# Kernel tuning notes

Hardware: AMD Instinct MI355X
Metric: run time of the kernel (lower is better)

The kernel has to match this reference:

```python
import jax, jax.numpy as jnp
import numpy as np
import math

HEAD_NUM = 16


def _split_qkv(qkv, head_num):
    # torch: rearrange(qkv, 'b t (d k h) -> k b h t d', k=3, h=head_num)
    B, T, E3 = qkv.shape
    d = E3 // (3 * head_num)
    qkv = qkv.reshape(B, T, d, 3, head_num)        # (b,t,d,k,h)
    qkv = jnp.transpose(qkv, (3, 0, 4, 1, 2))       # (k,b,h,t,d)
    return qkv[0], qkv[1], qkv[2]


def setup_inputs() -> dict:
    key = jax.random.key(0)
    ks = jax.random.split(key, 6)
    B, T, E = 4, 1024, 1024
    return {
        "x": jax.random.normal(ks[0], (B, T, E), dtype=jnp.float32),
        "y": jax.random.normal(ks[1], (B, T, E), dtype=jnp.float32),
        "Wqkv1": jax.random.normal(ks[2], (3 * E, E), dtype=jnp.float32) * 0.02,
        "Wqkv2": jax.random.normal(ks[3], (3 * E, E), dtype=jnp.float32) * 0.02,
        "Wout1": jax.random.normal(ks[4], (E, E), dtype=jnp.float32) * 0.02,
        "Wout2": jax.random.normal(ks[5], (E, E), dtype=jnp.float32) * 0.02,
    }


def reference(x, y, Wqkv1, Wqkv2, Wout1, Wout2):
    B, T, E = x.shape
    H = HEAD_NUM
    dk = math.sqrt(E / H)

    qkv1 = x @ Wqkv1.T                              # (B,T,3E)
    qkv2 = y @ Wqkv2.T
    q1, k1, v1 = _split_qkv(qkv1, H)                # each (B,H,T,d)
    q2, k2, v2 = _split_qkv(qkv2, H)

    # cross attention: stream-2 queries attend to stream-1 keys/values and vice versa
    energy1 = jnp.einsum('bhid,bhjd->bhij', q2, k1) / dk
    energy2 = jnp.einsum('bhid,bhjd->bhij', q1, k2) / dk
    attn1 = jax.nn.softmax(energy1, axis=-1)
    attn2 = jax.nn.softmax(energy2, axis=-1)

    xo = jnp.einsum('bhij,bhjd->bhid', attn1, v1)   # (B,H,T,d)
    yo = jnp.einsum('bhij,bhjd->bhid', attn2, v2)
    xo = jnp.transpose(xo, (0, 2, 1, 3)).reshape(B, T, E)  # b t (h d)
    yo = jnp.transpose(yo, (0, 2, 1, 3)).reshape(B, T, E)

    return xo @ Wout1.T, yo @ Wout2.T
```

## Files before the change

kernel.cpp:

```cpp
#include <hip/hip_runtime.h>
#include <hip/hip_bf16.h>

typedef __hip_bfloat16 bf16;
typedef __attribute__((ext_vector_type(8))) short short8;
typedef __attribute__((ext_vector_type(4))) short short4v;
typedef __attribute__((ext_vector_type(4))) float f32x4;

#define MFMA_BF16(a, b, c) __builtin_amdgcn_mfma_f32_16x16x32_bf16((a), (b), (c), 0, 0, 0)

#define QSCALE 0.1803368860111270f

__device__ __forceinline__ short f2bf(float f) {
    union { bf16 h; short s; } u;
    u.h = __float2bfloat16(f);
    return u.s;
}

#if defined(__has_builtin) && __has_builtin(__builtin_amdgcn_cvt_pk_bf16_f32)
typedef __attribute__((ext_vector_type(2))) __bf16 bf16x2_t;
__device__ __forceinline__ unsigned int pk2(float a, float b) {
    union { bf16x2_t v; unsigned int u; } x;
    x.v = __builtin_amdgcn_cvt_pk_bf16_f32(a, b);
    return x.u;
}
#else
__device__ __forceinline__ unsigned int pk2(float a, float b) {
    union { bf16 h[2]; unsigned int u; } x;
    x.h[0] = __float2bfloat16(a);
    x.h[1] = __float2bfloat16(b);
    return x.u;
}
#endif

__device__ __forceinline__ void gload16(const void* g, void* l) {
    __builtin_amdgcn_global_load_lds(
        (const __attribute__((address_space(1))) unsigned int*)g,
        (__attribute__((address_space(3))) unsigned int*)l, 16, 0, 0);
}

__global__ void cvt_fused(const float* __restrict__ x, const float* __restrict__ y,
                          const float* __restrict__ wo1, const float* __restrict__ wo2,
                          const float* __restrict__ wq1, const float* __restrict__ wq2,
                          bf16* __restrict__ ox, bf16* __restrict__ oy,
                          bf16* __restrict__ oo1, bf16* __restrict__ oo2,
                          bf16* __restrict__ oq1, bf16* __restrict__ oq2) {
    const int yb = blockIdx.y;
    if (yb < 4) {
        int i = blockIdx.x * 256 + threadIdx.x;
        const float* src; bf16* dst; int n4;
        switch (yb) {
            case 0:  src = x;   dst = ox;  n4 = 1048576; break;
            case 1:  src = y;   dst = oy;  n4 = 1048576; break;
            case 2:  src = wo1; dst = oo1; n4 = 262144;  break;
            default: src = wo2; dst = oo2; n4 = 262144;  break;
        }
        if (i >= n4) return;
        float4 f = reinterpret_cast<const float4*>(src)[i];
        short4v s;
        s.x = f2bf(f.x); s.y = f2bf(f.y); s.z = f2bf(f.z); s.w = f2bf(f.w);
        reinterpret_cast<short4v*>(dst)[i] = s;
    } else {
        const int np = blockIdx.x;
        if (np >= 3072) return;
        const int comp = np >> 10, rem = np & 1023, h = rem >> 6, d = rem & 63;
        const int srow = d * 48 + comp * 16 + h;
        const float* src = ((yb == 5) ? wq2 : wq1) + (long)srow * 1024;
        bf16* dst = ((yb == 5) ? oq2 : oq1) + (long)np * 1024;
        const float sc = (comp == 0) ? QSCALE : 1.0f;
        int t = threadIdx.x;
        float4 f = reinterpret_cast<const float4*>(src)[t];
        short4v s;
        s.x = f2bf(f.x * sc); s.y = f2bf(f.y * sc); s.z = f2bf(f.z * sc); s.w = f2bf(f.w * sc);
        reinterpret_cast<short4v*>(dst)[t] = s;
    }
}

#define GATE4 do { asm volatile("s_waitcnt vmcnt(4)" ::: "memory"); \
    __builtin_amdgcn_s_barrier(); __builtin_amdgcn_sched_barrier(0); } while (0)

__global__ __launch_bounds__(512, 2)
void gemm_qkv256(const bf16* __restrict__ A0g, const bf16* __restrict__ B0g,
                 void* o0a, void* o0b, void* o0c,
                 const bf16* __restrict__ A1g, const bf16* __restrict__ B1g,
                 void* o1a, void* o1b, void* o1c) {
    extern __shared__ short smem[];
    const int z = blockIdx.z;
    const short* A = reinterpret_cast<const short*>(z ? A1g : A0g);
    const short* B = reinterpret_cast<const short*>(z ? B1g : B0g);
    const int tid  = threadIdx.x;
    const int lane = tid & 63;
    const int w    = tid >> 6;
    const int quad = lane >> 4;
    const int l16  = lane & 15;
    const long M0 = (long)blockIdx.y * 256;
    const long N0 = (long)blockIdx.x * 256;

    const int rowblk = (w >> 2) * 64;
    const int colblk = (w & 3) * 32;
    const int cA0  = (quad ^ (l16 & 7)) * 8;
    const int aoff = (rowblk + l16) * 64;
    const int boff = 16384 + (colblk + l16) * 64;
    const int w512 = w * 512;

    const short* Asrc = A + (M0 + w * 8 + (lane >> 3)) * 1024 + ((lane & 7) ^ (lane >> 3)) * 8;
    const short* Bsrc = B + (N0 + w * 8 + (lane >> 3)) * 1024 + ((lane & 7) ^ (lane >> 3)) * 8;

    f32x4 acc[4][4][2] = {};
    short8 af[4][2], bfv[2][2];

#define SA256(half, tt, nbase) do { \
    const short* _s = Asrc + (half) * 131072 + (tt) * 64; \
    short* _d = smem + (nbase) + (half) * 8192 + w512; \
    gload16(_s, _d); gload16(_s + 65536, _d + 4096); } while (0)
#define SB256(half, tt, nbase) do { \
    const short* _s = Bsrc + (half) * 131072 + (tt) * 64; \
    short* _d = smem + (nbase) + 16384 + (half) * 8192 + w512; \
    gload16(_s, _d); gload16(_s + 65536, _d + 4096); } while (0)
#define RDA256(Ah, bbv) do { \
    _Pragma("unroll") for (int mt = 0; mt < 4; ++mt) { \
        const short* _p = &smem[(bbv) + (Ah) * 8192 + aoff + mt * 1024]; \
        af[mt][0] = *reinterpret_cast<const short8*>(_p + cA0); \
        af[mt][1] = *reinterpret_cast<const short8*>(_p + (cA0 ^ 32)); } } while (0)
#define RDB256(Bh, bbv) do { \
    _Pragma("unroll") for (int nt = 0; nt < 2; ++nt) { \
        const short* _p = &smem[(bbv) + (Bh) * 8192 + boff + nt * 1024]; \
        bfv[nt][0] = *reinterpret_cast<const short8*>(_p + cA0); \
        bfv[nt][1] = *reinterpret_cast<const short8*>(_p + (cA0 ^ 32)); } } while (0)
#define MM256(p) do { \
    __builtin_amdgcn_s_setprio(1); \
    _Pragma("unroll") for (int mt = 0; mt < 4; ++mt) \
    _Pragma("unroll") for (int nt = 0; nt < 2; ++nt) { \
        acc[p][mt][nt] = MFMA_BF16(af[mt][0], bfv[nt][0], acc[p][mt][nt]); \
        acc[p][mt][nt] = MFMA_BF16(af[mt][1], bfv[nt][1], acc[p][mt][nt]); } \
    __builtin_amdgcn_s_setprio(0); } while (0)

    SA256(0, 0, 0); SB256(0, 0, 0); SB256(1, 0, 0); SA256(1, 0, 0);

#pragma unroll 1
    for (int t = 0; t < 15; ++t) {
        const int bb = (t & 1) << 15;
        const int nb = bb ^ 32768;
        GATE4;
        SA256(0, t + 1, nb);
        RDA256(0, bb); RDB256(0, bb);
        __builtin_amdgcn_sched_barrier(0);
        MM256(0);
        GATE4;
        SB256(0, t + 1, nb);
        RDB256(1, bb);
        __builtin_amdgcn_sched_barrier(0);
        MM256(1);
        GATE4;
        SB256(1, t + 1, nb);
        RDA256(1, bb); RDB256(0, bb);
        __builtin_amdgcn_sched_barrier(0);
        MM256(2);
        SA256(1, t + 1, nb);
        RDB256(1, bb);
        __builtin_amdgcn_sched_barrier(0);
        MM256(3);
    }
    asm volatile("s_waitcnt vmcnt(0)" ::: "memory");
    __builtin_amdgcn_s_barrier();
    __builtin_amdgcn_sched_barrier(0);
    {
        const int bb = 32768;
        RDA256(0, bb); RDB256(0, bb); MM256(0);
        RDB256(1, bb); MM256(1);
        RDA256(1, bb); RDB256(0, bb); MM256(2);
        RDB256(1, bb); MM256(3);
    }

    if (blockIdx.x < 8) {
        short* dst = reinterpret_cast<short*>(blockIdx.x < 4 ? (z ? o1a : o0a)
                                                             : (z ? o1b : o0b));
        const int b = (int)(M0 >> 10);
        const int t00 = ((int)M0 & 1023);
        const int hd00 = ((int)blockIdx.x & 3) * 256;
#pragma unroll
        for (int p = 0; p < 4; ++p) {
            const int Ah = p >> 1, Bh = p & 1;
            const int tr0 = t00 + Ah * 128 + rowblk + quad * 4;
#pragma unroll
            for (int nt = 0; nt < 2; ++nt) {
                const int hd = hd00 + Bh * 128 + colblk + nt * 16 + l16;
                const int h = hd >> 6, d = hd & 63;
                short* dp = dst + (long)(b * 16 + h) * 65536 + d;
#pragma unroll
                for (int mt = 0; mt < 4; ++mt)
#pragma unroll
                    for (int r = 0; r < 4; ++r)
                        dp[(long)(tr0 + mt * 16 + r) * 64] = f2bf(acc[p][mt][nt][r]);
            }
        }
    } else {
        short* vT = reinterpret_cast<short*>(z ? o1c : o0c);
        const int b = (int)(M0 >> 10);
        const int hd00 = ((int)blockIdx.x - 8) * 256;
        short* ws = smem + w * 2304;
        const int c8 = (lane & 7) * 8;
        const int colr = lane >> 3;
#pragma unroll
        for (int p = 0; p < 4; ++p) {
            const int Ah = p >> 1, Bh = p & 1;
#pragma unroll
            for (int nt = 0; nt < 2; ++nt)
#pragma unroll
                for (int mt = 0; mt < 4; ++mt) {
                    uint2 uu;
                    uu.x = pk2(acc[p][mt][nt][0], acc[p][mt][nt][1]);
                    uu.y = pk2(acc[p][mt][nt][2], acc[p][mt][nt][3]);
                    *reinterpret_cast<uint2*>(&ws[(nt * 16 + l16) * 72 + mt * 16 + quad * 4]) = uu;
                }
            const int tb = ((int)M0 & 1023) + Ah * 128 + rowblk + c8;
#pragma unroll
            for (int q4 = 0; q4 < 4; ++q4) {
                const int col = q4 * 8 + colr;
                const int hd = hd00 + Bh * 128 + colblk + col;
                const int h = hd >> 6, d = hd & 63;
                short8 v = *reinterpret_cast<const short8*>(&ws[col * 72 + c8]);
                *reinterpret_cast<short8*>(&vT[(long)(b * 16 + h) * 65536 + (long)d * 1024 + tb]) = v;
            }
        }
    }
#undef SA256
#undef SB256
#undef RDA256
#undef RDB256
#undef MM256
}

template <int MODE>
__global__ __launch_bounds__(256)
void gemm_k(const bf16* __restrict__ A0g, const bf16* __restrict__ B0g,
            void* o0a, void* o0b, void* o0c,
            const bf16* __restrict__ A1g, const bf16* __restrict__ B1g,
            void* o1a, void* o1b, void* o1c, int N) {
    __shared__ short smem2[20480];
    const int z = blockIdx.z;
    const short* A = reinterpret_cast<const short*>(z ? A1g : A0g);
    const short* B = reinterpret_cast<const short*>(z ? B1g : B0g);
    const int tid  = threadIdx.x;
    const int lane = tid & 63;
    const int w    = tid >> 6;
    const int wr   = w >> 1;
    const int wc   = w & 1;
    const int quad = lane >> 4;
    const int l16  = lane & 15;
    const long bM = (long)blockIdx.y * 128;

    f32x4 acc[4][4] = {};

    const int sr  = lane >> 2;
    const int scs = ((lane & 3) ^ (sr & 3)) * 8;
    const short* Ag0 = A + (bM + 32 * w + sr) * 1024 + scs;
    const short* Ag1 = Ag0 + 16 * 1024;
    const short* Bg0 = B + ((long)blockIdx.x * 128 + 32 * w + sr) * 1024 + scs;
    const short* Bg1 = Bg0 + 16 * 1024;
    const int sq = (quad ^ (l16 & 3)) * 8;

    {
        short* sb = smem2;
        gload16(Ag0, sb + w * 1024);
        gload16(Ag1, sb + w * 1024 + 512);
        gload16(Bg0, sb + 4096 + w * 1024);
        gload16(Bg1, sb + 4096 + w * 1024 + 512);
    }
    __syncthreads();

    for (int iter = 0; iter < 32; ++iter) {
        const int cur = iter & 1;
        if (iter < 31) {
            const int koff = (iter + 1) * 32;
            short* sb = smem2 + (cur ^ 1) * 8192;
            gload16(Ag0 + koff, sb + w * 1024);
            gload16(Ag1 + koff, sb + w * 1024 + 512);
            gload16(Bg0 + koff, sb + 4096 + w * 1024);
            gload16(Bg1 + koff, sb + 4096 + w * 1024 + 512);
        }
        const short* Ab = smem2 + cur * 8192;
        const short* Bb = Ab + 4096;

        short8 af[4], bfr[4];
#pragma unroll
        for (int mt = 0; mt < 4; ++mt)
            af[mt] = *reinterpret_cast<const short8*>(&Ab[(wr * 64 + mt * 16 + l16) * 32 + sq]);
#pragma unroll
        for (int nt = 0; nt < 4; ++nt)
            bfr[nt] = *reinterpret_cast<const short8*>(&Bb[(wc * 64 + nt * 16 + l16) * 32 + sq]);
#pragma unroll
        for (int mt = 0; mt < 4; ++mt)
#pragma unroll
            for (int nt = 0; nt < 4; ++nt)
                acc[mt][nt] = MFMA_BF16(af[mt], bfr[nt], acc[mt][nt]);

        __syncthreads();
    }

    if (MODE == 1) {
        float* C = reinterpret_cast<float*>(z ? o1a : o0a);
        const long crow = bM + wr * 64 + quad * 4;
        const long ccol = (long)blockIdx.x * 128 + wc * 64 + l16;
#pragma unroll
        for (int mt = 0; mt < 4; ++mt)
#pragma unroll
            for (int nt = 0; nt < 4; ++nt)
#pragma unroll
                for (int r = 0; r < 4; ++r)
                    C[(crow + mt * 16 + r) * (long)N + ccol + nt * 16] = acc[mt][nt][r];
        return;
    }
    if (blockIdx.x < 16) {
        short* dst = reinterpret_cast<short*>(blockIdx.x >= 8 ? (z ? o1b : o0b)
                                                              : (z ? o1a : o0a));
        const int hd0 = (int)(blockIdx.x & 7) * 128 + wc * 64;
        const int b = (int)(bM >> 10);
        const int t0 = ((int)bM & 1023) + wr * 64 + quad * 4;
#pragma unroll
        for (int nt = 0; nt < 4; ++nt) {
            const int hd = hd0 + nt * 16 + l16;
            const int h = hd >> 6, d = hd & 63;
            short* dp = dst + ((long)(b * 16 + h) * 1024) * 64 + d;
#pragma unroll
            for (int mt = 0; mt < 4; ++mt)
#pragma unroll
                for (int r = 0; r < 4; ++r)
                    dp[(long)(t0 + mt * 16 + r) * 64] = f2bf(acc[mt][nt][r]);
        }
    }
}

__global__ __launch_bounds__(256)
void attn_kernel(const bf16* __restrict__ q0g, const bf16* __restrict__ k0g,
                 const bf16* __restrict__ v0g, bf16* __restrict__ o0g,
                 const bf16* __restrict__ q1g, const bf16* __restrict__ k1g,
                 const bf16* __restrict__ v1g, bf16* __restrict__ o1g) {
    __shared__ short smem[16384];
    const int bh = blockIdx.x;
    const int qt = blockIdx.y;
    const int z = blockIdx.z;
    const int b = bh >> 4, h = bh & 15;
    const int tid = threadIdx.x, lane = tid & 63, w = tid >> 6;
    const int quad = lane >> 4, l16 = lane & 15;

    const short* Qb = reinterpret_cast<const short*>(z ? q1g : q0g) + (long)bh * 1024 * 64;
    const short* Kb = reinterpret_cast<const short*>(z ? k1g : k0g) + (long)bh * 1024 * 64;
    const short* Vb = reinterpret_cast<const short*>(z ? v1g : v0g) + (long)bh * 64 * 1024;
    short* Ob = reinterpret_cast<short*>(z ? o1g : o0g);

    short8 qb[2][2];
#pragma unroll
    for (int qg = 0; qg < 2; ++qg) {
        const short* Qp = Qb + (long)(qt * 128 + qg * 64 + w * 16 + l16) * 64;
        qb[qg][0] = *reinterpret_cast<const short8*>(Qp + quad * 8);
        qb[qg][1] = *reinterpret_cast<const short8*>(Qp + 32 + quad * 8);
    }

    const int r8  = lane >> 3;
    const int sc0 = ((lane & 7) ^ (r8 & 3)) * 8;
    const short* Kg0 = Kb + (long)(16 * w + r8) * 64 + sc0;
    const short* Kg1 = Kb + (long)(16 * w + 8 + r8) * 64 + (sc0 ^ 32);
    const short* Vg0 = Vb + (long)(16 * w + r8) * 1024 + sc0;
    const short* Vg1 = Vb + (long)(16 * w + 8 + r8) * 1024 + (sc0 ^ 32);

    const int jbase = 8 * (l16 >> 2) + (l16 & 3);
    const int fKs = (l16 & 3) | (((l16 >> 2) & 1) << 2);
    const int s0  = (quad ^ fKs) * 8;
    const int fVs = (l16 & 3) | (((l16 >> 3) & 1) << 2);
    const int sv  = (quad ^ fVs) * 8;

    f32x4 o[2][4] = {};
    float li[2] = {0.f, 0.f};

    gload16(Kg0, smem + w * 1024); gload16(Kg1, smem + w * 1024 + 512);
    gload16(Vg0, smem + 4096 + w * 1024); gload16(Vg1, smem + 4096 + w * 1024 + 512);

#pragma unroll 1
    for (int iter = 0; iter < 16; ++iter) {
        const int cur = iter & 1;
        short* sb = smem + (cur ^ 1) * 8192;
        const bool pre = iter < 15;
        if (pre) {
            const long ko = (long)(iter + 1) * 4096;
            gload16(Kg0 + ko, sb + w * 1024);
            gload16(Kg1 + ko, sb + w * 1024 + 512);
        }
        if (pre) { asm volatile("s_waitcnt vmcnt(4)" ::: "memory"); }
        else     { asm volatile("s_waitcnt vmcnt(2)" ::: "memory"); }
        __builtin_amdgcn_s_barrier();
        __builtin_amdgcn_sched_barrier(0);

        const short* Ks = smem + cur * 8192;
        const short* Vs = Ks + 4096;

        f32x4 st[2][4];
        __builtin_amdgcn_s_setprio(1);
#pragma unroll
        for (int g = 0; g < 4; ++g) {
            const int goff = (g >> 1) * 32 + (g & 1) * 4;
            const short* kr = Ks + (jbase + goff) * 64;
            short8 k0 = *reinterpret_cast<const short8*>(kr + s0);
            short8 k1 = *reinterpret_cast<const short8*>(kr + (s0 ^ 32));
#pragma unroll
            for (int qg = 0; qg < 2; ++qg) {
                f32x4 zf = {0.f, 0.f, 0.f, 0.f};
                zf = MFMA_BF16(k0, qb[qg][0], zf);
                zf = MFMA_BF16(k1, qb[qg][1], zf);
                st[qg][g] = zf;
            }
        }
        __builtin_amdgcn_s_setprio(0);

        if (pre) {
            const long vo = (long)(iter + 1) * 64;
            gload16(Vg0 + vo, sb + 4096 + w * 1024);
            gload16(Vg1 + vo, sb + 4096 + w * 1024 + 512);
        }

        union { unsigned int u[4]; short8 s; } f0[2], f1[2];
#pragma unroll
        for (int qg = 0; qg < 2; ++qg) {
            float p[4][4];
            float rs = 0.f;
#pragma unroll
            for (int g = 0; g < 4; ++g)
#pragma unroll
                for (int r = 0; r < 4; ++r) {
                    float e = exp2f(st[qg][g][r]);
                    p[g][r] = e;
                    rs += e;
                }
            li[qg] += rs;
            f0[qg].u[0] = pk2(p[0][0], p[0][1]); f0[qg].u[1] = pk2(p[0][2], p[0][3]);
            f0[qg].u[2] = pk2(p[1][0], p[1][1]); f0[qg].u[3] = pk2(p[1][2], p[1][3]);
            f1[qg].u[0] = pk2(p[2][0], p[2][1]); f1[qg].u[1] = pk2(p[2][2], p[2][3]);
            f1[qg].u[2] = pk2(p[3][0], p[3][1]); f1[qg].u[3] = pk2(p[3][2], p[3][3]);
        }

        if (pre) { asm volatile("s_waitcnt vmcnt(4)" ::: "memory"); }
        else     { asm volatile("s_waitcnt vmcnt(0)" ::: "memory"); }
        __builtin_amdgcn_s_barrier();
        __builtin_amdgcn_sched_barrier(0);

        __builtin_amdgcn_s_setprio(1);
#pragma unroll
        for (int dt = 0; dt < 4; ++dt) {
            const short* vr = Vs + (dt * 16 + l16) * 64;
            short8 v0 = *reinterpret_cast<const short8*>(vr + sv);
            short8 v1 = *reinterpret_cast<const short8*>(vr + (sv ^ 32));
#pragma unroll
            for (int qg = 0; qg < 2; ++qg) {
                o[qg][dt] = MFMA_BF16(v0, f0[qg].s, o[qg][dt]);
                o[qg][dt] = MFMA_BF16(v1, f1[qg].s, o[qg][dt]);
            }
        }
        __builtin_amdgcn_s_setprio(0);
    }

    __syncthreads();

#pragma unroll
    for (int qg = 0; qg < 2; ++qg) {
        li[qg] += __shfl_xor(li[qg], 16);
        li[qg] += __shfl_xor(li[qg], 32);
    }

#pragma unroll
    for (int qg = 0; qg < 2; ++qg) {
        short* Os = smem + qg * 5120 + w * 1280;
        const float rl = 1.0f / li[qg];
#pragma unroll
        for (int dt = 0; dt < 4; ++dt) {
            uint2 uu;
            uu.x = pk2(o[qg][dt][0] * rl, o[qg][dt][1] * rl);
            uu.y = pk2(o[qg][dt][2] * rl, o[qg][dt][3] * rl);
            *reinterpret_cast<uint2*>(&Os[l16 * 80 + dt * 16 + quad * 4]) = uu;
        }
#pragma unroll
        for (int p = 0; p < 2; ++p) {
            int row = p * 8 + (lane >> 3);
            int ch = (lane & 7) * 8;
            short8 v = *reinterpret_cast<const short8*>(&Os[row * 80 + ch]);
            *reinterpret_cast<short8*>(&Ob[((long)(b * 1024) + qt * 128 + qg * 64 + w * 16 + row) * 1024 + h * 64 + ch]) = v;
        }
    }
}

extern "C" void kernel_launch(void* const* d_in, const int* in_sizes, int n_in,
                              void* d_out, int out_size, void* d_ws, size_t ws_size,
                              hipStream_t stream) {
    const float* x     = (const float*)d_in[0];
    const float* y     = (const float*)d_in[1];
    const float* Wqkv1 = (const float*)d_in[2];
    const float* Wqkv2 = (const float*)d_in[3];
    const float* Wout1 = (const float*)d_in[4];
    const float* Wout2 = (const float*)d_in[5];

    char* ws = (char*)d_ws;
    bf16* Wqkv1b = (bf16*)(ws + 0);
    bf16* Wqkv2b = (bf16*)(ws + 6291456);
    bf16* Wout1b = (bf16*)(ws + 12582912);
    bf16* Wout2b = (bf16*)(ws + 14680064);
    bf16* xb     = (bf16*)(ws + 16777216);
    bf16* yb     = (bf16*)(ws + 25165824);
    bf16* q1     = (bf16*)(ws + 33554432);
    bf16* k1     = (bf16*)(ws + 41943040);
    bf16* v1T    = (bf16*)(ws + 50331648);
    bf16* q2     = (bf16*)(ws + 58720256);
    bf16* k2     = (bf16*)(ws + 67108864);
    bf16* v2T    = (bf16*)(ws + 75497472);
    bf16* xo     = xb;
    bf16* yo     = yb;

    static bool s_attr = false;
    if (!s_attr) {
        (void)hipFuncSetAttribute(reinterpret_cast<const void*>(&gemm_qkv256),
                                  hipFuncAttributeMaxDynamicSharedMemorySize, 131072);
        s_attr = true;
    }

    cvt_fused<<<dim3(4096, 6), 256, 0, stream>>>(x, y, Wout1, Wout2, Wqkv1, Wqkv2,
                                                 xb, yb, Wout1b, Wout2b, Wqkv1b, Wqkv2b);

    gemm_qkv256<<<dim3(12, 16, 2), 512, 131072, stream>>>(xb, Wqkv1b, q1, k1, v1T,
                                                          yb, Wqkv2b, q2, k2, v2T);

    attn_kernel<<<dim3(64, 8, 2), 256, 0, stream>>>(q2, k1, v1T, xo,
                                                    q1, k2, v2T, yo);

    gemm_k<1><<<dim3(8, 32, 2), 256, 0, stream>>>(xo, Wout1b, (float*)d_out, nullptr, nullptr,
                                                  yo, Wout2b, ((float*)d_out) + 4194304, nullptr, nullptr,
                                                  1024);
}
```

Measured before the change: 263.9 us.

## Switch attention and output GEMM to triple-buffered LDS with one barrier per iteration

Both the attention kernel and the output-projection GEMM move from double-buffered LDS with two sync points per loop to a three-slot ring buffer. Each iteration now issues the next tile's loads first, waits on the previous ones and uses a single barrier. The three slots let the prefetch target a buffer no wave is still reading, which removes the trailing __syncthreads. The GEMM's MFMA block also gets raised priority, and exp2f is replaced with the hardware exp2 builtin. The cost is 50% more shared memory per block, which may lower occupancy.

```diff
diff --git a/kernel.cpp b/kernel.cpp
--- a/kernel.cpp
+++ b/kernel.cpp
@@ -30,6 +30,12 @@
     x.h[1] = __float2bfloat16(b);
     return x.u;
 }
+#endif
+
+#if defined(__has_builtin) && __has_builtin(__builtin_amdgcn_exp2f)
+#define EXP2F(x) __builtin_amdgcn_exp2f(x)
+#else
+#define EXP2F(x) exp2f(x)
 #endif
 
 __device__ __forceinline__ void gload16(const void* g, void* l) {
@@ -230,13 +236,10 @@
 #undef MM256
 }
 
-template <int MODE>
 __global__ __launch_bounds__(256)
-void gemm_k(const bf16* __restrict__ A0g, const bf16* __restrict__ B0g,
-            void* o0a, void* o0b, void* o0c,
-            const bf16* __restrict__ A1g, const bf16* __restrict__ B1g,
-            void* o1a, void* o1b, void* o1c, int N) {
-    __shared__ short smem2[20480];
+void gemm_out(const bf16* __restrict__ A0g, const bf16* __restrict__ B0g, float* __restrict__ C0,
+              const bf16* __restrict__ A1g, const bf16* __restrict__ B1g, float* __restrict__ C1) {
+    __shared__ short smem2[24576];
     const int z = blockIdx.z;
     const short* A = reinterpret_cast<const short*>(z ? A1g : A0g);
     const short* B = reinterpret_cast<const short*>(z ? B1g : B0g);
@@ -266,19 +269,26 @@
         gload16(Bg0, sb + 4096 + w * 1024);
         gload16(Bg1, sb + 4096 + w * 1024 + 512);
     }
-    __syncthreads();
-
+
+    int bcur = 0;
+#pragma unroll 1
     for (int iter = 0; iter < 32; ++iter) {
-        const int cur = iter & 1;
+        int bnext = bcur + 1; if (bnext == 3) bnext = 0;
         if (iter < 31) {
             const int koff = (iter + 1) * 32;
-            short* sb = smem2 + (cur ^ 1) * 8192;
+            short* sb = smem2 + bnext * 8192;
             gload16(Ag0 + koff, sb + w * 1024);
             gload16(Ag1 + koff, sb + w * 1024 + 512);
             gload16(Bg0 + koff, sb + 4096 + w * 1024);
             gload16(Bg1 + koff, sb + 4096 + w * 1024 + 512);
-        }
-        const short* Ab = smem2 + cur * 8192;
+            asm volatile("s_waitcnt vmcnt(4)" ::: "memory");
+        } else {
+            asm volatile("s_waitcnt vmcnt(0)" ::: "memory");
+        }
+        __builtin_amdgcn_s_barrier();
+        __builtin_amdgcn_sched_barrier(0);
+
+        const short* Ab = smem2 + bcur * 8192;
         const short* Bb = Ab + 4096;
 
         short8 af[4], bfr[4];
@@ -288,46 +298,26 @@
 #pragma unroll
         for (int nt = 0; nt < 4; ++nt)
             bfr[nt] = *reinterpret_cast<const short8*>(&Bb[(wc * 64 + nt * 16 + l16) * 32 + sq]);
+        __builtin_amdgcn_s_setprio(1);
 #pragma unroll
         for (int mt = 0; mt < 4; ++mt)
 #pragma unroll
             for (int nt = 0; nt < 4; ++nt)
                 acc[mt][nt] = MFMA_BF16(af[mt], bfr[nt], acc[mt][nt]);
-
-        __syncthreads();
-    }
-
-    if (MODE == 1) {
-        float* C = reinterpret_cast<float*>(z ? o1a : o0a);
-        const long crow = bM + wr * 64 + quad * 4;
-        const long ccol = (long)blockIdx.x * 128 + wc * 64 + l16;
-#pragma unroll
-        for (int mt = 0; mt < 4; ++mt)
-#pragma unroll
-            for (int nt = 0; nt < 4; ++nt)
-#pragma unroll
-                for (int r = 0; r < 4; ++r)
-                    C[(crow + mt * 16 + r) * (long)N + ccol + nt * 16] = acc[mt][nt][r];
-        return;
-    }
-    if (blockIdx.x < 16) {
-        short* dst = reinterpret_cast<short*>(blockIdx.x >= 8 ? (z ? o1b : o0b)
-                                                              : (z ? o1a : o0a));
-        const int hd0 = (int)(blockIdx.x & 7) * 128 + wc * 64;
-        const int b = (int)(bM >> 10);
-        const int t0 = ((int)bM & 1023) + wr * 64 + quad * 4;
-#pragma unroll
-        for (int nt = 0; nt < 4; ++nt) {
-            const int hd = hd0 + nt * 16 + l16;
-            const int h = hd >> 6, d = hd & 63;
-            short* dp = dst + ((long)(b * 16 + h) * 1024) * 64 + d;
-#pragma unroll
-            for (int mt = 0; mt < 4; ++mt)
-#pragma unroll
-                for (int r = 0; r < 4; ++r)
-                    dp[(long)(t0 + mt * 16 + r) * 64] = f2bf(acc[mt][nt][r]);
-        }
-    }
+        __builtin_amdgcn_s_setprio(0);
+        bcur = bnext;
+    }
+
+    float* C = z ? C1 : C0;
+    const long crow = bM + wr * 64 + quad * 4;
+    const long ccol = (long)blockIdx.x * 128 + wc * 64 + l16;
+#pragma unroll
+    for (int mt = 0; mt < 4; ++mt)
+#pragma unroll
+        for (int nt = 0; nt < 4; ++nt)
+#pragma unroll
+            for (int r = 0; r < 4; ++r)
+                C[(crow + mt * 16 + r) * 1024L + ccol + nt * 16] = acc[mt][nt][r];
 }
 
 __global__ __launch_bounds__(256)
@@ -335,7 +325,7 @@
                  const bf16* __restrict__ v0g, bf16* __restrict__ o0g,
                  const bf16* __restrict__ q1g, const bf16* __restrict__ k1g,
                  const bf16* __restrict__ v1g, bf16* __restrict__ o1g) {
-    __shared__ short smem[16384];
+    __shared__ short smem[24576];
     const int bh = blockIdx.x;
     const int qt = blockIdx.y;
     const int z = blockIdx.z;
@@ -375,22 +365,26 @@
     gload16(Kg0, smem + w * 1024); gload16(Kg1, smem + w * 1024 + 512);
     gload16(Vg0, smem + 4096 + w * 1024); gload16(Vg1, smem + 4096 + w * 1024 + 512);
 
+    int bcur = 0;
 #pragma unroll 1
     for (int iter = 0; iter < 16; ++iter) {
-        const int cur = iter & 1;
-        short* sb = smem + (cur ^ 1) * 8192;
-        const bool pre = iter < 15;
-        if (pre) {
+        int bnext = bcur + 1; if (bnext == 3) bnext = 0;
+        if (iter < 15) {
+            short* sb = smem + bnext * 8192;
             const long ko = (long)(iter + 1) * 4096;
+            const long vo = (long)(iter + 1) * 64;
             gload16(Kg0 + ko, sb + w * 1024);
             gload16(Kg1 + ko, sb + w * 1024 + 512);
-        }
-        if (pre) { asm volatile("s_waitcnt vmcnt(4)" ::: "memory"); }
-        else     { asm volatile("s_waitcnt vmcnt(2)" ::: "memory"); }
+            gload16(Vg0 + vo, sb + 4096 + w * 1024);
+            gload16(Vg1 + vo, sb + 4096 + w * 1024 + 512);
+            asm volatile("s_waitcnt vmcnt(4)" ::: "memory");
+        } else {
+            asm volatile("s_waitcnt vmcnt(0)" ::: "memory");
+        }
         __builtin_amdgcn_s_barrier();
         __builtin_amdgcn_sched_barrier(0);
 
-        const short* Ks = smem + cur * 8192;
+        const short* Ks = smem + bcur * 8192;
         const short* Vs = Ks + 4096;
 
         f32x4 st[2][4];
@@ -411,12 +405,6 @@
         }
         __builtin_amdgcn_s_setprio(0);
 
-        if (pre) {
-            const long vo = (long)(iter + 1) * 64;
-            gload16(Vg0 + vo, sb + 4096 + w * 1024);
-            gload16(Vg1 + vo, sb + 4096 + w * 1024 + 512);
-        }
-
         union { unsigned int u[4]; short8 s; } f0[2], f1[2];
 #pragma unroll
         for (int qg = 0; qg < 2; ++qg) {
@@ -426,7 +414,7 @@
             for (int g = 0; g < 4; ++g)
 #pragma unroll
                 for (int r = 0; r < 4; ++r) {
-                    float e = exp2f(st[qg][g][r]);
+                    float e = EXP2F(st[qg][g][r]);
                     p[g][r] = e;
                     rs += e;
                 }
@@ -437,11 +425,6 @@
             f1[qg].u[2] = pk2(p[3][0], p[3][1]); f1[qg].u[3] = pk2(p[3][2], p[3][3]);
         }
 
-        if (pre) { asm volatile("s_waitcnt vmcnt(4)" ::: "memory"); }
-        else     { asm volatile("s_waitcnt vmcnt(0)" ::: "memory"); }
-        __builtin_amdgcn_s_barrier();
-        __builtin_amdgcn_sched_barrier(0);
-
         __builtin_amdgcn_s_setprio(1);
 #pragma unroll
         for (int dt = 0; dt < 4; ++dt) {
@@ -455,6 +438,7 @@
             }
         }
         __builtin_amdgcn_s_setprio(0);
+        bcur = bnext;
     }
 
     __syncthreads();
@@ -528,7 +512,6 @@
     attn_kernel<<<dim3(64, 8, 2), 256, 0, stream>>>(q2, k1, v1T, xo,
                                                     q1, k2, v2T, yo);
 
-    gemm_k<1><<<dim3(8, 32, 2), 256, 0, stream>>>(xo, Wout1b, (float*)d_out, nullptr, nullptr,
-                                                  yo, Wout2b, ((float*)d_out) + 4194304, nullptr, nullptr,
-                                                  1024);
-}
+    gemm_out<<<dim3(8, 32, 2), 256, 0, stream>>>(xo, Wout1b, (float*)d_out,
+                                                 yo, Wout2b, ((float*)d_out) + 4194304);
+}
```

Result: faster. 241.9 us (-8.3%).
